# Kernel optimization log

Hardware: AMD Instinct MI355X
Metric: run time of the kernel (lower is better)

The kernel has to match this reference:

```python
import jax, jax.numpy as jnp
import numpy as np

B, S, D = 2, 8192, 1024
H, HD, FD = 16, 64, 256

def setup_inputs() -> dict:
    key = jax.random.key(0)
    ks = jax.random.split(key, 6)
    sc = 1.0 / np.sqrt(D)
    return {
        "hidden_states": jax.random.normal(ks[0], (B, S, D), jnp.float32),
        "Wq": jax.random.normal(ks[1], (D, D), jnp.float32) * sc,
        "Wk": jax.random.normal(ks[2], (D, D), jnp.float32) * sc,
        "Wv": jax.random.normal(ks[3], (D, D), jnp.float32) * sc,
        "Wo": jax.random.normal(ks[4], (D, D), jnp.float32) * sc,
        "Wf": jax.random.normal(ks[5], (FD, HD), jnp.float32) * (1.0 / np.sqrt(HD)),
    }

def reference(hidden_states, Wq, Wk, Wv, Wo, Wf):
    b, s, _ = hidden_states.shape
    # projections (torch Linear: x @ W.T), split heads -> (b, s, h, hd)
    q = (hidden_states @ Wq.T).reshape(b, s, H, HD)
    k = (hidden_states @ Wk.T).reshape(b, s, H, HD)
    v = (hidden_states @ Wv.T).reshape(b, s, H, HD)
    # elu+1 feature map -> (b, s, h, f)
    qf = jax.nn.elu(q @ Wf.T) + 1.0
    kf = jax.nn.elu(k @ Wf.T) + 1.0
    # global kv summary: (b, h, f, d)
    kv = jnp.einsum('bshf,bshd->bhfd', kf, v)
    out = jnp.einsum('bshf,bhfd->bshd', qf, kv)
    k_sum = kf.sum(axis=1)                       # (b, h, f)
    norm = jnp.einsum('bshf,bhf->bsh', qf, k_sum)[..., None] + 1e-6
    out = (out / norm).reshape(b, s, D)
    return out @ Wo.T
```

## Files before the change

kernel.cpp:

```cpp
#include <hip/hip_runtime.h>
#include <stdint.h>

typedef __bf16 bf16_t;
typedef __attribute__((ext_vector_type(8))) __bf16 bfv8;
typedef __attribute__((ext_vector_type(4))) __bf16 bfv4;
typedef __attribute__((ext_vector_type(4))) float f32x4;

constexpr int BATCH = 2, SEQ = 8192, DIM = 1024, NH = 16, HDIM = 64, FDIM = 256;
constexpr int MROWS = BATCH * SEQ;
constexpr int NCHUNK = 16;
constexpr int KV_NIT = (SEQ / NCHUNK) / 32;
constexpr int KVP_CH = 32 * 256 * 68;

__device__ __forceinline__ f32x4 mfma_bf16(bfv8 a, bfv8 b, f32x4 c) {
  return __builtin_amdgcn_mfma_f32_16x16x32_bf16(a, b, c, 0, 0, 0);
}

__device__ __forceinline__ void gload_lds16(const bf16_t* g, bf16_t* lds) {
  auto const* gp = reinterpret_cast<const __attribute__((address_space(1))) uint32_t*>(
      reinterpret_cast<uintptr_t>(g));
  auto* lp = reinterpret_cast<__attribute__((address_space(3))) uint32_t*>(
      reinterpret_cast<uintptr_t>(lds));
  __builtin_amdgcn_global_load_lds(gp, lp, 16, 0, 0);
}

__device__ __forceinline__ void stage128x64(const bf16_t* g_base, int k0,
                                            bf16_t* lds, int wid, int lane) {
#pragma unroll
  for (int j = 0; j < 4; ++j) {
    int r0 = (wid * 4 + j) * 8;
    int g_row = r0 + (lane >> 3);
    int g_slot = (lane & 7) ^ (g_row & 7);
    const bf16_t* src = g_base + (size_t)g_row * DIM + k0 + g_slot * 8;
    gload_lds16(src, lds + r0 * 64);
  }
}

__global__ __launch_bounds__(256) void cvt_all(const float* __restrict__ X,
                                               const float* __restrict__ Wq,
                                               const float* __restrict__ Wk,
                                               const float* __restrict__ Wv,
                                               const float* __restrict__ Wo,
                                               const float* __restrict__ Wf,
                                               bf16_t* __restrict__ Xb,
                                               bf16_t* __restrict__ W3,
                                               bf16_t* __restrict__ Wob,
                                               bf16_t* __restrict__ Wfb) {
  int i = blockIdx.x * 256 + threadIdx.x;
  const float* src;
  bf16_t* dst;
  int off;
  if (i < 4194304) {
    src = X; dst = Xb; off = i;
  } else {
    int j = i - 4194304;
    if (j < 786432) {
      int seg = j >> 18;
      off = j & 262143;
      src = (seg == 0) ? Wq : ((seg == 1) ? Wk : Wv);
      dst = W3 + (size_t)seg * 1048576;
    } else if (j < 1048576) {
      off = j - 786432; src = Wo; dst = Wob;
    } else {
      off = j - 1048576; src = Wf; dst = Wfb;
    }
  }
  float4 v = reinterpret_cast<const float4*>(src)[off];
  bfv4 o = {(__bf16)v.x, (__bf16)v.y, (__bf16)v.z, (__bf16)v.w};
  reinterpret_cast<bfv4*>(dst)[off] = o;
}

__global__ __launch_bounds__(256) void gemm_qkv(const bf16_t* __restrict__ A,
                                                const bf16_t* __restrict__ Wall,
                                                bf16_t* __restrict__ Q,
                                                bf16_t* __restrict__ K,
                                                bf16_t* __restrict__ V) {
  __shared__ bf16_t As[128 * 64];
  __shared__ bf16_t Bs[128 * 64];
  int z = blockIdx.z;
  const bf16_t* Wm = Wall + (size_t)z * (DIM * DIM);
  bf16_t* C = (z == 0) ? Q : ((z == 1) ? K : V);
  int lane = threadIdx.x & 63, wid = threadIdx.x >> 6;
  int lr = lane & 15, lg = lane >> 4;
  int wr = wid >> 1, wc = wid & 1;
  int brow = blockIdx.x * 128, bcol = blockIdx.y * 128;
  const bf16_t* Ab = A + (size_t)brow * DIM;
  const bf16_t* Bb = Wm + (size_t)bcol * DIM;
  f32x4 acc[4][4] = {};
  for (int ks = 0; ks < DIM / 64; ++ks) {
    stage128x64(Ab, ks * 64, As, wid, lane);
    stage128x64(Bb, ks * 64, Bs, wid, lane);
    __syncthreads();
#pragma unroll
    for (int kk = 0; kk < 2; ++kk) {
      bfv8 af[4], bg[4];
#pragma unroll
      for (int t = 0; t < 4; ++t) {
        int ar = wr * 64 + t * 16 + lr;
        af[t] = *reinterpret_cast<const bfv8*>(&As[ar * 64 + (((kk * 4 + lg) ^ (ar & 7)) * 8)]);
        int br = wc * 64 + t * 16 + lr;
        bg[t] = *reinterpret_cast<const bfv8*>(&Bs[br * 64 + (((kk * 4 + lg) ^ (br & 7)) * 8)]);
      }
#pragma unroll
      for (int i = 0; i < 4; ++i)
#pragma unroll
        for (int j = 0; j < 4; ++j) acc[i][j] = mfma_bf16(af[i], bg[j], acc[i][j]);
    }
    __syncthreads();
  }
#pragma unroll
  for (int i = 0; i < 4; ++i) {
    int r = brow + wr * 64 + i * 16 + lg * 4;
#pragma unroll
    for (int j = 0; j < 4; ++j) {
      int c = bcol + wc * 64 + j * 16 + lr;
#pragma unroll
      for (int q = 0; q < 4; ++q) C[(size_t)(r + q) * DIM + c] = (__bf16)acc[i][j][q];
    }
  }
}

__global__ __launch_bounds__(256) void gemm_final(const bf16_t* __restrict__ A,
                                                  const bf16_t* __restrict__ W,
                                                  float* __restrict__ C) {
  __shared__ bf16_t As[128 * 64];
  __shared__ bf16_t Bs[128 * 64];
  int lane = threadIdx.x & 63, wid = threadIdx.x >> 6;
  int lr = lane & 15, lg = lane >> 4;
  int wr = wid >> 1, wc = wid & 1;
  int brow = blockIdx.x * 128, bcol = blockIdx.y * 128;
  const bf16_t* Ab = A + (size_t)brow * DIM;
  const bf16_t* Bb = W + (size_t)bcol * DIM;
  f32x4 acc[4][4] = {};
  for (int ks = 0; ks < DIM / 64; ++ks) {
    stage128x64(Ab, ks * 64, As, wid, lane);
    stage128x64(Bb, ks * 64, Bs, wid, lane);
    __syncthreads();
#pragma unroll
    for (int kk = 0; kk < 2; ++kk) {
      bfv8 af[4], bg[4];
#pragma unroll
      for (int t = 0; t < 4; ++t) {
        int ar = wr * 64 + t * 16 + lr;
        af[t] = *reinterpret_cast<const bfv8*>(&As[ar * 64 + (((kk * 4 + lg) ^ (ar & 7)) * 8)]);
        int br = wc * 64 + t * 16 + lr;
        bg[t] = *reinterpret_cast<const bfv8*>(&Bs[br * 64 + (((kk * 4 + lg) ^ (br & 7)) * 8)]);
      }
#pragma unroll
      for (int i = 0; i < 4; ++i)
#pragma unroll
        for (int j = 0; j < 4; ++j) acc[i][j] = mfma_bf16(af[i], bg[j], acc[i][j]);
    }
    __syncthreads();
  }
#pragma unroll
  for (int i = 0; i < 4; ++i) {
    int r = brow + wr * 64 + i * 16 + lg * 4;
#pragma unroll
    for (int j = 0; j < 4; ++j) {
      int c = bcol + wc * 64 + j * 16 + lr;
#pragma unroll
      for (int q = 0; q < 4; ++q) C[(size_t)(r + q) * DIM + c] = acc[i][j][q];
    }
  }
}

__global__ __launch_bounds__(256, 2) void kv_fused(const bf16_t* __restrict__ Kb,
                                                   const bf16_t* __restrict__ Vb,
                                                   const bf16_t* __restrict__ Wf,
                                                   float* __restrict__ kv_part) {
  __shared__ bf16_t kf_lds[4][64 * 36];
  __shared__ bf16_t vt[2][80 * 36];
  int chunk = blockIdx.x, bh = blockIdx.y;
  int b = bh >> 4, h = bh & 15;
  int lane = threadIdx.x & 63, wid = threadIdx.x >> 6;
  int lr = lane & 15, lg = lane >> 4;
  int f0 = wid * 64;
  for (int i = threadIdx.x; i < 2 * 16 * 36; i += 256) {
    int bufn = i / (16 * 36), rem = i % (16 * 36);
    int n = rem / 36, s = rem % 36;
    vt[bufn][(64 + n) * 36 + s] = (n == 0) ? (__bf16)1.0f : (__bf16)0.0f;
  }
  bfv8 wf[4][2];
#pragma unroll
  for (int ft = 0; ft < 4; ++ft)
#pragma unroll
    for (int kk = 0; kk < 2; ++kk)
      wf[ft][kk] = *reinterpret_cast<const bfv8*>(Wf + (size_t)(f0 + ft * 16 + lr) * HDIM + kk * 32 + lg * 8);
  int si = threadIdx.x >> 3, c8 = threadIdx.x & 7;
  const bf16_t* Kbase = Kb + (size_t)b * SEQ * DIM + h * HDIM;
  const bf16_t* Vbase = Vb + (size_t)b * SEQ * DIM + h * HDIM;
  int s0 = chunk * (SEQ / NCHUNK);

  bfv8 vv0 = *reinterpret_cast<const bfv8*>(Vbase + (size_t)(s0 + si) * DIM + c8 * 8);
  bfv8 vvA = *reinterpret_cast<const bfv8*>(Vbase + (size_t)(s0 + 32 + si) * DIM + c8 * 8);
  bfv8 vvB;
  bfv8 krgA[2][2], krgB[2][2];
#pragma unroll
  for (int st = 0; st < 2; ++st)
#pragma unroll
    for (int kk = 0; kk < 2; ++kk)
      krgA[st][kk] = *reinterpret_cast<const bfv8*>(Kbase + (size_t)(s0 + st * 16 + lr) * DIM + kk * 32 + lg * 8);
#pragma unroll
  for (int j = 0; j < 8; ++j) vt[0][(c8 * 8 + j) * 36 + si] = vv0[j];
  asm volatile("s_waitcnt lgkmcnt(0)" ::: "memory");
  __builtin_amdgcn_s_barrier();

  f32x4 acc[4][5] = {};

  auto STEP = [&](int it, bfv8(&krgC)[2][2], bfv8& vvC, bfv8(&krgN)[2][2], bfv8& vvN,
                  int cur) __attribute__((always_inline)) {
    int sbn = s0 + (it + 1) * 32;
    if (it + 1 < KV_NIT) {
#pragma unroll
      for (int st = 0; st < 2; ++st)
#pragma unroll
        for (int kk = 0; kk < 2; ++kk)
          krgN[st][kk] = *reinterpret_cast<const bfv8*>(Kbase + (size_t)(sbn + st * 16 + lr) * DIM + kk * 32 + lg * 8);
      if (it + 2 < KV_NIT)
        vvN = *reinterpret_cast<const bfv8*>(Vbase + (size_t)(sbn + 32 + si) * DIM + c8 * 8);
    }
    f32x4 ckf[4][2] = {};
#pragma unroll
    for (int ft = 0; ft < 4; ++ft)
#pragma unroll
      for (int st = 0; st < 2; ++st)
#pragma unroll
        for (int kk = 0; kk < 2; ++kk) ckf[ft][st] = mfma_bf16(wf[ft][kk], krgC[st][kk], ckf[ft][st]);
    if (it + 1 < KV_NIT) {
#pragma unroll
      for (int j = 0; j < 8; ++j) vt[cur ^ 1][(c8 * 8 + j) * 36 + si] = vvC[j];
    }
#pragma unroll
    for (int ft = 0; ft < 4; ++ft)
#pragma unroll
      for (int st = 0; st < 2; ++st)
#pragma unroll
        for (int q = 0; q < 4; ++q) {
          float x = ckf[ft][st][q];
          x = (x > 0.0f) ? (x + 1.0f) : __expf(x);
          kf_lds[wid][(ft * 16 + lg * 4 + q) * 36 + st * 16 + lr] = (__bf16)x;
        }
    bfv8 af[4], bg[5];
#pragma unroll
    for (int ft = 0; ft < 4; ++ft)
      af[ft] = *reinterpret_cast<const bfv8*>(&kf_lds[wid][(ft * 16 + lr) * 36 + lg * 8]);
#pragma unroll
    for (int nt = 0; nt < 5; ++nt)
      bg[nt] = *reinterpret_cast<const bfv8*>(&vt[cur][(nt * 16 + lr) * 36 + lg * 8]);
#pragma unroll
    for (int ft = 0; ft < 4; ++ft)
#pragma unroll
      for (int nt = 0; nt < 5; ++nt) acc[ft][nt] = mfma_bf16(af[ft], bg[nt], acc[ft][nt]);
    asm volatile("s_waitcnt lgkmcnt(0)" ::: "memory");
    __builtin_amdgcn_s_barrier();
  };

  for (int it2 = 0; it2 < KV_NIT; it2 += 2) {
    STEP(it2, krgA, vvA, krgB, vvB, 0);
    STEP(it2 + 1, krgB, vvB, krgA, vvA, 1);
  }

  float* outb = kv_part + ((size_t)chunk * 32 + bh) * (FDIM * 68);
#pragma unroll
  for (int ft = 0; ft < 4; ++ft)
#pragma unroll
    for (int q = 0; q < 4; ++q) {
      int f = f0 + ft * 16 + lg * 4 + q;
#pragma unroll
      for (int nt = 0; nt < 4; ++nt)
        outb[(size_t)f * 68 + nt * 16 + lr] = acc[ft][nt][q];
      if (lr < 4) outb[(size_t)f * 68 + 64 + lr] = acc[ft][4][q];
    }
}

__global__ __launch_bounds__(256) void kv_reduce(const float* __restrict__ part,
                                                 bf16_t* __restrict__ kvT) {
  int i = blockIdx.x * 256 + threadIdx.x;
  if (i < KVP_CH) {
    int n = i % 68;
    int t = i / 68;
    int f = t & 255, bh = t >> 8;
    float s = 0.0f;
#pragma unroll
    for (int c = 0; c < NCHUNK; ++c) s += part[(size_t)c * KVP_CH + i];
    int fs = ((((f >> 3) ^ (n & 7)) << 3) | (f & 7));
    kvT[((size_t)bh * 80 + n) * FDIM + fs] = (__bf16)s;
  } else {
    int j = i - KVP_CH;
    int f = j & 255;
    int t = j >> 8;
    int n = 68 + t % 12, bh = t / 12;
    kvT[((size_t)bh * 80 + n) * FDIM + f] = (__bf16)0.0f;
  }
}

__global__ __launch_bounds__(256) void attn_fused(const bf16_t* __restrict__ Qb,
                                                  const bf16_t* __restrict__ Wf,
                                                  const bf16_t* __restrict__ kvT,
                                                  bf16_t* __restrict__ outp) {
  __shared__ bf16_t qf_lds[64 * 264];
  __shared__ bf16_t kv_lds[80 * 256];
  int rb = blockIdx.x, h = blockIdx.y;
  int row0 = rb * 64;
  int bh = (row0 >> 13) * NH + h;
  int lane = threadIdx.x & 63, wid = threadIdx.x >> 6;
  int lr = lane & 15, lg = lane >> 4;
  int f0 = wid * 64;
  const bf16_t* kvTb = kvT + (size_t)bh * 80 * FDIM;
#pragma unroll
  for (int i = 0; i < 10; ++i) {
    int sbase = wid * 640 + i * 64;
    gload_lds16(kvTb + (size_t)(sbase + lane) * 8, kv_lds + sbase * 8);
  }
  bfv8 qa[4][2], wfb[4][2];
#pragma unroll
  for (int t = 0; t < 4; ++t)
#pragma unroll
    for (int kk = 0; kk < 2; ++kk) {
      qa[t][kk] = *reinterpret_cast<const bfv8*>(Qb + (size_t)(row0 + t * 16 + lr) * DIM + h * HDIM + kk * 32 + lg * 8);
      wfb[t][kk] = *reinterpret_cast<const bfv8*>(Wf + (size_t)(f0 + t * 16 + lr) * HDIM + kk * 32 + lg * 8);
    }
  f32x4 cq[4][4] = {};
#pragma unroll
  for (int rt = 0; rt < 4; ++rt)
#pragma unroll
    for (int ft = 0; ft < 4; ++ft)
#pragma unroll
      for (int kk = 0; kk < 2; ++kk) cq[rt][ft] = mfma_bf16(qa[rt][kk], wfb[ft][kk], cq[rt][ft]);
#pragma unroll
  for (int rt = 0; rt < 4; ++rt)
#pragma unroll
    for (int ft = 0; ft < 4; ++ft)
#pragma unroll
      for (int q = 0; q < 4; ++q) {
        float x = cq[rt][ft][q];
        x = (x > 0.0f) ? (x + 1.0f) : __expf(x);
        qf_lds[(size_t)(rt * 16 + lg * 4 + q) * 264 + f0 + ft * 16 + lr] = (__bf16)x;
      }
  __syncthreads();
  f32x4 acc[5] = {};
#pragma unroll
  for (int ks = 0; ks < 8; ++ks) {
    bfv8 a = *reinterpret_cast<const bfv8*>(&qf_lds[(size_t)(wid * 16 + lr) * 264 + ks * 32 + lg * 8]);
#pragma unroll
    for (int nt = 0; nt < 5; ++nt) {
      bfv8 bg = *reinterpret_cast<const bfv8*>(
          &kv_lds[(size_t)(nt * 16 + lr) * 256 + (((ks * 4 + lg) ^ (lr & 7)) * 8)]);
      acc[nt] = mfma_bf16(a, bg, acc[nt]);
    }
  }
  __syncthreads();
#pragma unroll
  for (int q = 0; q < 4; ++q) {
    float nrm = __shfl(acc[4][q], (lane & 48)) + 1e-6f;
    int row = wid * 16 + lg * 4 + q;
#pragma unroll
    for (int nt = 0; nt < 4; ++nt)
      qf_lds[(size_t)row * 264 + nt * 16 + lr] = (__bf16)(acc[nt][q] / nrm);
  }
  __syncthreads();
#pragma unroll
  for (int rep = 0; rep < 2; ++rep) {
    int id = rep * 256 + threadIdx.x;
    int row = id >> 3, c8 = id & 7;
    bfv8 v = *reinterpret_cast<const bfv8*>(&qf_lds[(size_t)row * 264 + c8 * 8]);
    *reinterpret_cast<bfv8*>(&outp[(size_t)(row0 + row) * DIM + h * HDIM + c8 * 8]) = v;
  }
}

extern "C" void kernel_launch(void* const* d_in, const int* in_sizes, int n_in,
                              void* d_out, int out_size, void* d_ws, size_t ws_size,
                              hipStream_t stream) {
  const float* X  = (const float*)d_in[0];
  const float* Wq = (const float*)d_in[1];
  const float* Wk = (const float*)d_in[2];
  const float* Wv = (const float*)d_in[3];
  const float* Wo = (const float*)d_in[4];
  const float* Wf = (const float*)d_in[5];
  float* out = (float*)d_out;
  char* ws = (char*)d_ws;
  const size_t MB = 1ull << 20;
  if (ws_size < 75 * MB) return;

  bf16_t* Xb  = (bf16_t*)(ws + 0 * MB);
  bf16_t* W3  = (bf16_t*)(ws + 32 * MB);
  bf16_t* Qb  = (bf16_t*)(ws + 38 * MB);
  bf16_t* Wob = (bf16_t*)(ws + 70 * MB);
  bf16_t* Wfb = (bf16_t*)(ws + 72 * MB);
  bf16_t* kvT = (bf16_t*)(ws + 73 * MB);
  float* kv_part = (float*)(ws + 0 * MB);
  bf16_t* outp = (bf16_t*)(ws + 0 * MB);
  bf16_t* Kb = (bf16_t*)d_out;
  bf16_t* Vb = Kb + (size_t)MROWS * DIM;

  cvt_all<<<20496, 256, 0, stream>>>(X, Wq, Wk, Wv, Wo, Wf, Xb, W3, Wob, Wfb);

  gemm_qkv<<<dim3(128, 8, 3), 256, 0, stream>>>(Xb, W3, Qb, Kb, Vb);
  kv_fused<<<dim3(NCHUNK, 32), 256, 0, stream>>>(Kb, Vb, Wfb, kv_part);
  kv_reduce<<<2560, 256, 0, stream>>>(kv_part, kvT);
  attn_fused<<<dim3(256, NH), 256, 0, stream>>>(Qb, Wfb, kvT, outp);
  gemm_final<<<dim3(128, 8), 256, 0, stream>>>(outp, Wob, out);
}
```

Measured before the change: 301.0 us.

## Give each wave a private V-transpose tile to drop block barriers in kv_fused

Each of the four waves now loads and transposes its own copy of the 32x64 V tile into a per-wave LDS buffer, so the per-iteration block-wide barrier and the shared double-buffered V staging go away. This removes cross-wave synchronisation stalls in the KV accumulation loop. In exchange every wave issues four times the V global loads and LDS transpose writes, and the V loads are no longer prefetched an iteration ahead, so their latency is exposed within each step.

```diff
diff --git a/kernel.cpp b/kernel.cpp
--- a/kernel.cpp
+++ b/kernel.cpp
@@ -170,16 +170,15 @@
                                                    const bf16_t* __restrict__ Wf,
                                                    float* __restrict__ kv_part) {
   __shared__ bf16_t kf_lds[4][64 * 36];
-  __shared__ bf16_t vt[2][80 * 36];
+  __shared__ bf16_t vt[4][80 * 36];
   int chunk = blockIdx.x, bh = blockIdx.y;
   int b = bh >> 4, h = bh & 15;
   int lane = threadIdx.x & 63, wid = threadIdx.x >> 6;
   int lr = lane & 15, lg = lane >> 4;
   int f0 = wid * 64;
-  for (int i = threadIdx.x; i < 2 * 16 * 36; i += 256) {
-    int bufn = i / (16 * 36), rem = i % (16 * 36);
-    int n = rem / 36, s = rem % 36;
-    vt[bufn][(64 + n) * 36 + s] = (n == 0) ? (__bf16)1.0f : (__bf16)0.0f;
+  for (int i = lane; i < 16 * 36; i += 64) {
+    int n = i / 36, s = i - n * 36;
+    vt[wid][(64 + n) * 36 + s] = (n == 0) ? (__bf16)1.0f : (__bf16)0.0f;
   }
   bfv8 wf[4][2];
 #pragma unroll
@@ -187,38 +186,33 @@
 #pragma unroll
     for (int kk = 0; kk < 2; ++kk)
       wf[ft][kk] = *reinterpret_cast<const bfv8*>(Wf + (size_t)(f0 + ft * 16 + lr) * HDIM + kk * 32 + lg * 8);
-  int si = threadIdx.x >> 3, c8 = threadIdx.x & 7;
   const bf16_t* Kbase = Kb + (size_t)b * SEQ * DIM + h * HDIM;
   const bf16_t* Vbase = Vb + (size_t)b * SEQ * DIM + h * HDIM;
   int s0 = chunk * (SEQ / NCHUNK);
 
-  bfv8 vv0 = *reinterpret_cast<const bfv8*>(Vbase + (size_t)(s0 + si) * DIM + c8 * 8);
-  bfv8 vvA = *reinterpret_cast<const bfv8*>(Vbase + (size_t)(s0 + 32 + si) * DIM + c8 * 8);
-  bfv8 vvB;
   bfv8 krgA[2][2], krgB[2][2];
 #pragma unroll
   for (int st = 0; st < 2; ++st)
 #pragma unroll
     for (int kk = 0; kk < 2; ++kk)
       krgA[st][kk] = *reinterpret_cast<const bfv8*>(Kbase + (size_t)(s0 + st * 16 + lr) * DIM + kk * 32 + lg * 8);
-#pragma unroll
-  for (int j = 0; j < 8; ++j) vt[0][(c8 * 8 + j) * 36 + si] = vv0[j];
-  asm volatile("s_waitcnt lgkmcnt(0)" ::: "memory");
-  __builtin_amdgcn_s_barrier();
 
   f32x4 acc[4][5] = {};
 
-  auto STEP = [&](int it, bfv8(&krgC)[2][2], bfv8& vvC, bfv8(&krgN)[2][2], bfv8& vvN,
-                  int cur) __attribute__((always_inline)) {
-    int sbn = s0 + (it + 1) * 32;
+  auto STEP = [&](int it, bfv8(&krgC)[2][2], bfv8(&krgN)[2][2]) __attribute__((always_inline)) {
+    int sb = s0 + it * 32;
+    bfv8 vv[4];
+#pragma unroll
+    for (int rep = 0; rep < 4; ++rep) {
+      int idx = rep * 64 + lane;
+      vv[rep] = *reinterpret_cast<const bfv8*>(Vbase + (size_t)(sb + (idx >> 3)) * DIM + (idx & 7) * 8);
+    }
     if (it + 1 < KV_NIT) {
 #pragma unroll
       for (int st = 0; st < 2; ++st)
 #pragma unroll
         for (int kk = 0; kk < 2; ++kk)
-          krgN[st][kk] = *reinterpret_cast<const bfv8*>(Kbase + (size_t)(sbn + st * 16 + lr) * DIM + kk * 32 + lg * 8);
-      if (it + 2 < KV_NIT)
-        vvN = *reinterpret_cast<const bfv8*>(Vbase + (size_t)(sbn + 32 + si) * DIM + c8 * 8);
+          krgN[st][kk] = *reinterpret_cast<const bfv8*>(Kbase + (size_t)(sb + 32 + st * 16 + lr) * DIM + kk * 32 + lg * 8);
     }
     f32x4 ckf[4][2] = {};
 #pragma unroll
@@ -227,9 +221,11 @@
       for (int st = 0; st < 2; ++st)
 #pragma unroll
         for (int kk = 0; kk < 2; ++kk) ckf[ft][st] = mfma_bf16(wf[ft][kk], krgC[st][kk], ckf[ft][st]);
-    if (it + 1 < KV_NIT) {
-#pragma unroll
-      for (int j = 0; j < 8; ++j) vt[cur ^ 1][(c8 * 8 + j) * 36 + si] = vvC[j];
+#pragma unroll
+    for (int rep = 0; rep < 4; ++rep) {
+      int idx = rep * 64 + lane;
+#pragma unroll
+      for (int j = 0; j < 8; ++j) vt[wid][((idx & 7) * 8 + j) * 36 + (idx >> 3)] = vv[rep][j];
     }
 #pragma unroll
     for (int ft = 0; ft < 4; ++ft)
@@ -247,18 +243,16 @@
       af[ft] = *reinterpret_cast<const bfv8*>(&kf_lds[wid][(ft * 16 + lr) * 36 + lg * 8]);
 #pragma unroll
     for (int nt = 0; nt < 5; ++nt)
-      bg[nt] = *reinterpret_cast<const bfv8*>(&vt[cur][(nt * 16 + lr) * 36 + lg * 8]);
+      bg[nt] = *reinterpret_cast<const bfv8*>(&vt[wid][(nt * 16 + lr) * 36 + lg * 8]);
 #pragma unroll
     for (int ft = 0; ft < 4; ++ft)
 #pragma unroll
       for (int nt = 0; nt < 5; ++nt) acc[ft][nt] = mfma_bf16(af[ft], bg[nt], acc[ft][nt]);
-    asm volatile("s_waitcnt lgkmcnt(0)" ::: "memory");
-    __builtin_amdgcn_s_barrier();
   };
 
   for (int it2 = 0; it2 < KV_NIT; it2 += 2) {
-    STEP(it2, krgA, vvA, krgB, vvB, 0);
-    STEP(it2 + 1, krgB, vvB, krgA, vvA, 1);
+    STEP(it2, krgA, krgB);
+    STEP(it2 + 1, krgB, krgA);
   }
 
   float* outb = kv_part + ((size_t)chunk * 32 + bh) * (FDIM * 68);
```

New measurement: 301.0 us. Within noise of the previous version (+0.0%).
